# Performance work log

Measured on AMD Instinct MI355X. Metric: run time of the kernel, lower is better.

## Reference

```python
import jax, jax.numpy as jnp
import numpy as np

B, C, H, W = 16, 128, 112, 112
OUTC = 256


def _conv(x, w, padding, groups=1, bias=None):
    y = jax.lax.conv_general_dilated(
        x, w, window_strides=(1, 1), padding=[(padding, padding), (padding, padding)],
        dimension_numbers=("NCHW", "OIHW", "NCHW"), feature_group_count=groups)
    if bias is not None:
        y = y + bias[None, :, None, None]
    return y


def _grid_sample_1ch(chan, g):
    # chan: [B,H,W] single channel; g: [B,H,W,2] with (x,y) in [-1,1].
    # PyTorch grid_sample: bilinear, zeros padding, align_corners=False.
    Bn, Hc, Wc = chan.shape
    ix = (g[..., 0] + 1.0) * (Wc * 0.5) - 0.5
    iy = (g[..., 1] + 1.0) * (Hc * 0.5) - 0.5
    x0 = jnp.floor(ix)
    y0 = jnp.floor(iy)
    wx = ix - x0
    wy = iy - y0
    x0i = x0.astype(jnp.int32)
    y0i = y0.astype(jnp.int32)
    flat = chan.reshape(Bn, -1)

    def gather(yi, xi):
        valid = (yi >= 0) & (yi < Hc) & (xi >= 0) & (xi < Wc)
        idx = jnp.clip(yi, 0, Hc - 1) * Wc + jnp.clip(xi, 0, Wc - 1)
        v = jnp.take_along_axis(flat, idx.reshape(Bn, -1), axis=1).reshape(idx.shape)
        return jnp.where(valid, v, 0.0)

    v00 = gather(y0i, x0i)
    v01 = gather(y0i, x0i + 1)
    v10 = gather(y0i + 1, x0i)
    v11 = gather(y0i + 1, x0i + 1)
    return (v00 * (1 - wx) * (1 - wy) + v01 * wx * (1 - wy)
            + v10 * (1 - wx) * wy + v11 * wx * wy)


def setup_inputs() -> dict:
    key = jax.random.key(0)
    k1, k2, k3, k4 = jax.random.split(key, 4)
    x = jax.random.normal(k1, (B, C, H, W), dtype=jnp.float32)
    depth_w = jax.random.normal(k2, (C, 1, 3, 3), dtype=jnp.float32) * 0.1
    point_w = jax.random.normal(k3, (OUTC, C, 1, 1), dtype=jnp.float32) * 0.05
    offset_w = jax.random.normal(k4, (2 * C, C, 3, 3), dtype=jnp.float32) * 0.02
    offset_b = jnp.zeros((2 * C,), dtype=jnp.float32)
    return {"x": x, "depth_w": depth_w, "point_w": point_w,
            "offset_w": offset_w, "offset_b": offset_b}


def reference(x, depth_w, point_w, offset_w, offset_b):
    offset = jnp.tanh(_conv(x, offset_w, padding=1, bias=offset_b))  # [B,2C,H,W]
    out = _conv(x, depth_w, padding=1, groups=C)                     # [B,C,H,W]

    # Base grid, matching np.meshgrid + np.repeat([C,C], axis=0):
    # channels 0..C-1 are all X, channels C..2C-1 are all Y.
    gX, gY = jnp.meshgrid(jnp.linspace(-1.0, 1.0, W), jnp.linspace(-1.0, 1.0, H), indexing="xy")
    grid = jnp.concatenate([gX[None], gY[None]], axis=0)  # [2,H,W]
    grid = jnp.repeat(grid, C, axis=0)                    # [2C,H,W]

    sg = jnp.clip(grid[None] + offset, -1.0, 1.0)         # [B,2C,H,W]
    sg = sg.transpose(0, 2, 3, 1)                         # [B,H,W,2C]
    sg = sg.reshape(B, H, W, C, 2).transpose(3, 0, 1, 2, 4)  # [C,B,H,W,2]

    chans = out.transpose(1, 0, 2, 3)                     # [C,B,H,W]
    sampled = jax.vmap(_grid_sample_1ch)(chans, sg)       # [C,B,H,W]
    sampled = sampled.transpose(1, 0, 2, 3)               # [B,C,H,W]

    return _conv(sampled, point_w, padding=0)             # [B,OUTC,H,W]
```

## Files before the change

### kernel.cpp

```cpp
#include <hip/hip_runtime.h>
#include <hip/hip_bf16.h>

#define B_    16
#define C_    128
#define H_    112
#define W_    112
#define OUTC_ 256
#define TWOC_ 256
#define HW_   (H_ * W_)
#define CHW_  ((size_t)C_ * HW_)
#define PH_   114
#define PW_   114
#define PHW_  (PH_ * PW_)

typedef __hip_bfloat16 bf16;
typedef short bf16x8 __attribute__((ext_vector_type(8)));
typedef short s16x4  __attribute__((ext_vector_type(4)));
typedef float f32x4  __attribute__((ext_vector_type(4)));

__device__ __forceinline__ float b2f(bf16 v) { return __bfloat162float(v); }
__device__ __forceinline__ bf16  f2b(float v) { return __float2bfloat16(v); }

__device__ __forceinline__ float rd(const float* p) { return *p; }
__device__ __forceinline__ float rd(const bf16* p)  { return b2f(*p); }
__device__ __forceinline__ void  wr(float* p, float v) { *p = v; }
__device__ __forceinline__ void  wr(bf16* p,  float v) { *p = f2b(v); }

__device__ __forceinline__ float fast_tanh(float v) {
    float e = __expf(2.f * v);
    return 1.f - 2.f / (e + 1.f);
}

__global__ __launch_bounds__(256) void k_probe(const unsigned short* __restrict__ x,
                                               int* __restrict__ flag) {
    __shared__ int cnt[256];
    int tid = threadIdx.x;
    int c = 0;
#pragma unroll
    for (int i = 0; i < 8; ++i) {
        unsigned short u = x[tid * 8 + i];
        int e = (u >> 7) & 0xFF;
        if (e >= 135) c++;
    }
    cnt[tid] = c;
    __syncthreads();
    if (tid == 0) {
        int s = 0;
        for (int i = 0; i < 256; ++i) s += cnt[i];
        *flag = (s > 64) ? 1 : 0;
    }
}

template <typename TI>
__device__ void pad_body(const TI* __restrict__ x, float* __restrict__ xp) {
    size_t idx = (size_t)blockIdx.x * 256 + threadIdx.x;
    const size_t total = (size_t)B_ * C_ * PHW_;
    if (idx >= total) return;
    int pc  = (int)(idx / PHW_);
    int rem = (int)(idx - (size_t)pc * PHW_);
    int ph = rem / PW_;
    int pw = rem - ph * PW_;
    int h = ph - 1, w = pw - 1;
    float v = 0.f;
    if (h >= 0 && h < H_ && w >= 0 && w < W_)
        v = rd(x + (size_t)pc * HW_ + h * W_ + w);
    xp[idx] = v;
}

__global__ __launch_bounds__(256) void k_pad(const void* x, float* xp, const int* flag) {
    if (*flag) pad_body<float>((const float*)x, xp);
    else       pad_body<bf16>((const bf16*)x, xp);
}

__global__ __launch_bounds__(256) void k_wprep(const void* __restrict__ ow,
                                               bf16* __restrict__ wth,
                                               bf16* __restrict__ wtl,
                                               const int* __restrict__ flag) {
    int i = blockIdx.x * 256 + threadIdx.x;
    if (i >= 9 * 4 * 256 * 32) return;
    int cp  = i & 31;
    int oc  = (i >> 5) & 255;
    int tcc = i >> 13;
    int cc  = tcc & 3;
    int tap = tcc >> 2;
    int c   = cc * 32 + cp;
    size_t src = ((size_t)oc * C_ + c) * 9 + tap;
    float v = (*flag) ? ((const float*)ow)[src] : b2f(((const bf16*)ow)[src]);
    bf16 hb = f2b(v);
    float lo = v - b2f(hb);
    wth[i] = hb;
    wtl[i] = f2b(lo);
}

__global__ __launch_bounds__(256) void k_offset_mfma(
    const float* __restrict__ xp, const bf16* __restrict__ wth,
    const bf16* __restrict__ wtl, const void* __restrict__ ob,
    float* __restrict__ off, const int* __restrict__ flag)
{
    __shared__ alignas(16) short Sh[PH_ * 32];
    __shared__ alignas(16) short Sl[PH_ * 32];

    const int tid  = threadIdx.x;
    const int lane = tid & 63;
    const int wv   = tid >> 6;
    const int l15  = lane & 15;
    const int l4   = lane >> 4;
    const int hraw = blockIdx.x;
    const int h    = (hraw & 7) * 14 + (hraw >> 3);
    const int b    = blockIdx.y;
    const int fullp = *flag;

    f32x4 acc[4][7];
    f32x4 zero = {0.f, 0.f, 0.f, 0.f};
#pragma unroll
    for (int m = 0; m < 4; ++m)
#pragma unroll
        for (int n = 0; n < 7; ++n) acc[m][n] = zero;

    for (int cc = 0; cc < 4; ++cc) {
        for (int kh = 0; kh < 3; ++kh) {
            __syncthreads();
            for (int i = tid; i < 912; i += 256) {
                int n  = i % 114;
                int cq = i / 114;
                const float* src = xp + ((size_t)(b * C_ + cc * 32 + cq * 4)) * PHW_
                                      + (size_t)(h + kh) * PW_ + n;
                short hs[4], ls[4];
#pragma unroll
                for (int t = 0; t < 4; ++t) {
                    float v = src[(size_t)t * PHW_];
                    bf16 hb = f2b(v);
                    float hv = b2f(hb);
                    bf16 lb = f2b(v - hv);
                    hs[t] = *(short*)&hb;
                    ls[t] = *(short*)&lb;
                }
                int ob_ = (cq * 8) ^ (((n >> 1) & 3) << 4);
                int so  = n * 32 + (ob_ >> 1);
                s16x4 th, tl;
                th[0] = hs[0]; th[1] = hs[1]; th[2] = hs[2]; th[3] = hs[3];
                tl[0] = ls[0]; tl[1] = ls[1]; tl[2] = ls[2]; tl[3] = ls[3];
                *(s16x4*)&Sh[so] = th;
                *(s16x4*)&Sl[so] = tl;
            }
            __syncthreads();

            for (int kw = 0; kw < 3; ++kw) {
                const size_t wchunk = ((size_t)((kh * 3 + kw) * 4 + cc)) * (256 * 32);
                bf16x8 ah[4], al[4];
#pragma unroll
                for (int m = 0; m < 4; ++m) {
                    size_t aoff = (size_t)(wv * 64 + m * 16 + l15) * 32 + 8 * l4;
                    ah[m] = *(const bf16x8*)(wth + wchunk + aoff);
                }
                if (fullp) {
#pragma unroll
                    for (int m = 0; m < 4; ++m) {
                        size_t aoff = (size_t)(wv * 64 + m * 16 + l15) * 32 + 8 * l4;
                        al[m] = *(const bf16x8*)(wtl + wchunk + aoff);
                    }
                }
#pragma unroll
                for (int n = 0; n < 7; ++n) {
                    int rowb = n * 16 + l15 + kw;
                    int o2   = (16 * l4) ^ (((rowb >> 1) & 3) << 4);
                    int so   = rowb * 32 + (o2 >> 1);
                    bf16x8 xh = *(const bf16x8*)&Sh[so];
#pragma unroll
                    for (int m = 0; m < 4; ++m)
                        acc[m][n] = __builtin_amdgcn_mfma_f32_16x16x32_bf16(
                            ah[m], xh, acc[m][n], 0, 0, 0);
                    if (fullp) {
                        bf16x8 xl = *(const bf16x8*)&Sl[so];
#pragma unroll
                        for (int m = 0; m < 4; ++m)
                            acc[m][n] = __builtin_amdgcn_mfma_f32_16x16x32_bf16(
                                ah[m], xl, acc[m][n], 0, 0, 0);
#pragma unroll
                        for (int m = 0; m < 4; ++m)
                            acc[m][n] = __builtin_amdgcn_mfma_f32_16x16x32_bf16(
                                al[m], xh, acc[m][n], 0, 0, 0);
                    }
                }
            }
        }
    }

#pragma unroll
    for (int m = 0; m < 4; ++m) {
        int ocb = wv * 64 + m * 16 + l4 * 4;
        float bias[4];
#pragma unroll
        for (int j = 0; j < 4; ++j)
            bias[j] = fullp ? ((const float*)ob)[ocb + j]
                            : b2f(((const bf16*)ob)[ocb + j]);
#pragma unroll
        for (int n = 0; n < 7; ++n) {
            int w = n * 16 + l15;
#pragma unroll
            for (int j = 0; j < 4; ++j) {
                size_t o = ((size_t)(b * TWOC_ + ocb + j)) * HW_ + (size_t)h * W_ + w;
                off[o] = fast_tanh(acc[m][n][j] + bias[j]);
            }
        }
    }
}

template <typename TI>
__device__ void dw_body(const TI* __restrict__ x, const TI* __restrict__ dw,
                        bf16* __restrict__ out) {
    int hw = blockIdx.x * 256 + threadIdx.x;
    int c = blockIdx.y, b = blockIdx.z;
    int h = hw / W_, w = hw - h * W_;
    float wv[9];
#pragma unroll
    for (int k = 0; k < 9; ++k) wv[k] = rd(dw + c * 9 + k);
    const TI* xc = x + (size_t)b * CHW_ + (size_t)c * HW_;
    float acc = 0.f;
#pragma unroll
    for (int kh = 0; kh < 3; ++kh) {
        int hh = h + kh - 1;
        bool hv = (hh >= 0) && (hh < H_);
#pragma unroll
        for (int kw = 0; kw < 3; ++kw) {
            int ww = w + kw - 1;
            bool v = hv && (ww >= 0) && (ww < W_);
            acc += (v ? rd(xc + hh * W_ + ww) : 0.f) * wv[kh * 3 + kw];
        }
    }
    out[(size_t)(b * C_ + c) * HW_ + hw] = f2b(acc);
}

__global__ __launch_bounds__(256) void k_dw(const void* x, const void* dw,
                                            bf16* out, const int* flag) {
    if (*flag) dw_body<float>((const float*)x, (const float*)dw, out);
    else       dw_body<bf16>((const bf16*)x, (const bf16*)dw, out);
}

__global__ __launch_bounds__(256) void k_sample(
    const float* __restrict__ off, const bf16* __restrict__ dwout,
    bf16* __restrict__ samp) {
    int hw = blockIdx.x * 256 + threadIdx.x;
    int c = blockIdx.y, b = blockIdx.z;
    int h = hw / W_, w = hw - h * W_;

    float gbase = (c < 64) ? (-1.f + 2.f * (float)w / 111.f)
                           : (-1.f + 2.f * (float)h / 111.f);
    const float* offb = off + (size_t)b * TWOC_ * HW_;
    float ox = offb[(size_t)(2 * c) * HW_ + hw];
    float oy = offb[(size_t)(2 * c + 1) * HW_ + hw];
    float gx = fminf(fmaxf(gbase + ox, -1.f), 1.f);
    float gy = fminf(fmaxf(gbase + oy, -1.f), 1.f);
    float ix = (gx + 1.f) * 56.f - 0.5f;
    float iy = (gy + 1.f) * 56.f - 0.5f;
    float x0f = floorf(ix), y0f = floorf(iy);
    float wx = ix - x0f, wy = iy - y0f;
    int x0 = (int)x0f, y0 = (int)y0f;

    const bf16* p = dwout + (size_t)(b * C_ + c) * HW_;
    float v00 = 0.f, v01 = 0.f, v10 = 0.f, v11 = 0.f;
    bool y0v = (y0 >= 0) && (y0 < H_), y1v = (y0 + 1 >= 0) && (y0 + 1 < H_);
    bool x0v = (x0 >= 0) && (x0 < W_), x1v = (x0 + 1 >= 0) && (x0 + 1 < W_);
    if (y0v && x0v) v00 = b2f(p[y0 * W_ + x0]);
    if (y0v && x1v) v01 = b2f(p[y0 * W_ + x0 + 1]);
    if (y1v && x0v) v10 = b2f(p[(y0 + 1) * W_ + x0]);
    if (y1v && x1v) v11 = b2f(p[(y0 + 1) * W_ + x0 + 1]);

    float v = v00 * (1.f - wx) * (1.f - wy) + v01 * wx * (1.f - wy)
            + v10 * (1.f - wx) * wy + v11 * wx * wy;
    samp[(size_t)(b * C_ + c) * HW_ + hw] = f2b(v);
}

#define PWT 8
template <typename TI, typename TO>
__device__ void pw_body(const bf16* __restrict__ samp, const TI* __restrict__ pw,
                        TO* __restrict__ out, float* pwl) {
    int tid = threadIdx.x;
    int ocg = blockIdx.y * PWT;
    for (int i = tid; i < C_ * PWT; i += 256) {
        int j = i / C_;
        int c = i - j * C_;
        pwl[c * PWT + j] = rd(pw + (size_t)(ocg + j) * C_ + c);
    }
    __syncthreads();

    int hw = blockIdx.x * 256 + tid;
    int b = blockIdx.z;
    const bf16* sp = samp + (size_t)b * C_ * HW_ + hw;
    float acc[PWT];
#pragma unroll
    for (int j = 0; j < PWT; ++j) acc[j] = 0.f;
    for (int c = 0; c < C_; ++c) {
        float v = b2f(sp[(size_t)c * HW_]);
        const float* wrp = pwl + c * PWT;
#pragma unroll
        for (int j = 0; j < PWT; ++j) acc[j] += v * wrp[j];
    }
    size_t ob = (size_t)b * OUTC_ * HW_ + (size_t)ocg * HW_ + hw;
#pragma unroll
    for (int j = 0; j < PWT; ++j) wr(out + ob + (size_t)j * HW_, acc[j]);
}

__global__ __launch_bounds__(256) void k_pw(const bf16* samp, const void* pw,
                                            void* out, const int* flag) {
    __shared__ float pwl[C_ * PWT];
    if (*flag) pw_body<float, float>(samp, (const float*)pw, (float*)out, pwl);
    else       pw_body<bf16, bf16>(samp, (const bf16*)pw, (bf16*)out, pwl);
}

extern "C" void kernel_launch(void* const* d_in, const int* in_sizes, int n_in,
                              void* d_out, int out_size, void* d_ws, size_t ws_size,
                              hipStream_t stream) {
    (void)in_sizes; (void)n_in; (void)out_size; (void)ws_size;
    const void* x        = d_in[0];
    const void* depth_w  = d_in[1];
    const void* point_w  = d_in[2];
    const void* offset_w = d_in[3];
    const void* offset_b = d_in[4];

    char* ws = (char*)d_ws;
    int*   flag = (int*)ws;
    float* xp   = (float*)(ws + 256);
    const size_t pad_bytes = (size_t)B_ * C_ * PHW_ * 4;
    const size_t off_bytes = (size_t)B_ * TWOC_ * HW_ * 4;
    float* off  = (float*)(ws + 256 + pad_bytes);
    bf16*  wth  = (bf16*)(ws + 256 + pad_bytes + off_bytes);
    bf16*  wtl  = wth + 9 * 4 * 256 * 32;
    bf16* dwout = (bf16*)(ws + 256);
    bf16* samp  = (bf16*)(ws + 256 + (size_t)B_ * C_ * HW_ * 2);

    const int pad_blocks = (int)(((size_t)B_ * C_ * PHW_ + 255) / 256);

    k_probe      <<<1, 256, 0, stream>>>((const unsigned short*)x, flag);
    k_wprep      <<<1152, 256, 0, stream>>>(offset_w, wth, wtl, flag);
    k_pad        <<<pad_blocks, 256, 0, stream>>>(x, xp, flag);
    k_offset_mfma<<<dim3(H_, B_), 256, 0, stream>>>(xp, wth, wtl, offset_b, off, flag);
    k_dw         <<<dim3(49, C_, B_),          256, 0, stream>>>(x, depth_w, dwout, flag);
    k_sample     <<<dim3(49, C_, B_),          256, 0, stream>>>(off, dwout, samp);
    k_pw         <<<dim3(49, OUTC_ / PWT, B_), 256, 0, stream>>>(samp, point_w, d_out, flag);
}
```

Before: 1.188 ms.

## Fuse bilinear sampling into an MFMA pointwise conv kernel per row

Merges the grid-sample and pointwise 1x1 conv kernels into one kernel per (row, batch). Each block samples all channels for a row into swizzled LDS, then runs the 128-to-256 channel matmul on bf16 MFMA using weights split into hi/lo parts that a new prep kernel builds. This removes the round trip of the sampled tensor through global memory and replaces scalar FMA loops with matrix cores. In exchange, the sampling gathers per block become less coalesced (channel-strided offset reads), and the output stores are scattered per lane.

After: 1.411 ms. 1.19x slower.

```diff
diff --git a/kernel.cpp b/kernel.cpp
--- a/kernel.cpp
+++ b/kernel.cpp
@@ -92,6 +92,24 @@
     wtl[i] = f2b(lo);
 }
 
+__global__ __launch_bounds__(256) void k_pwprep(const void* __restrict__ pw,
+                                                bf16* __restrict__ pwh,
+                                                bf16* __restrict__ pwl,
+                                                const int* __restrict__ flag) {
+    int i = blockIdx.x * 256 + threadIdx.x;
+    if (i >= 4 * 256 * 32) return;
+    int cp   = i & 31;
+    int oc   = (i >> 5) & 255;
+    int cc   = i >> 13;
+    int c    = cc * 32 + cp;
+    size_t src = (size_t)oc * C_ + c;
+    float v = (*flag) ? ((const float*)pw)[src] : b2f(((const bf16*)pw)[src]);
+    bf16 hb = f2b(v);
+    float lo = v - b2f(hb);
+    pwh[i] = hb;
+    pwl[i] = f2b(lo);
+}
+
 __global__ __launch_bounds__(256) void k_offset_mfma(
     const float* __restrict__ xp, const bf16* __restrict__ wth,
     const bf16* __restrict__ wtl, const void* __restrict__ ob,
@@ -237,75 +255,118 @@
     else       dw_body<bf16>((const bf16*)x, (const bf16*)dw, out);
 }
 
-__global__ __launch_bounds__(256) void k_sample(
+__global__ __launch_bounds__(256) void k_spw(
     const float* __restrict__ off, const bf16* __restrict__ dwout,
-    bf16* __restrict__ samp) {
-    int hw = blockIdx.x * 256 + threadIdx.x;
-    int c = blockIdx.y, b = blockIdx.z;
-    int h = hw / W_, w = hw - h * W_;
-
-    float gbase = (c < 64) ? (-1.f + 2.f * (float)w / 111.f)
-                           : (-1.f + 2.f * (float)h / 111.f);
-    const float* offb = off + (size_t)b * TWOC_ * HW_;
-    float ox = offb[(size_t)(2 * c) * HW_ + hw];
-    float oy = offb[(size_t)(2 * c + 1) * HW_ + hw];
-    float gx = fminf(fmaxf(gbase + ox, -1.f), 1.f);
-    float gy = fminf(fmaxf(gbase + oy, -1.f), 1.f);
-    float ix = (gx + 1.f) * 56.f - 0.5f;
-    float iy = (gy + 1.f) * 56.f - 0.5f;
-    float x0f = floorf(ix), y0f = floorf(iy);
-    float wx = ix - x0f, wy = iy - y0f;
-    int x0 = (int)x0f, y0 = (int)y0f;
-
-    const bf16* p = dwout + (size_t)(b * C_ + c) * HW_;
-    float v00 = 0.f, v01 = 0.f, v10 = 0.f, v11 = 0.f;
-    bool y0v = (y0 >= 0) && (y0 < H_), y1v = (y0 + 1 >= 0) && (y0 + 1 < H_);
-    bool x0v = (x0 >= 0) && (x0 < W_), x1v = (x0 + 1 >= 0) && (x0 + 1 < W_);
-    if (y0v && x0v) v00 = b2f(p[y0 * W_ + x0]);
-    if (y0v && x1v) v01 = b2f(p[y0 * W_ + x0 + 1]);
-    if (y1v && x0v) v10 = b2f(p[(y0 + 1) * W_ + x0]);
-    if (y1v && x1v) v11 = b2f(p[(y0 + 1) * W_ + x0 + 1]);
-
-    float v = v00 * (1.f - wx) * (1.f - wy) + v01 * wx * (1.f - wy)
-            + v10 * (1.f - wx) * wy + v11 * wx * wy;
-    samp[(size_t)(b * C_ + c) * HW_ + hw] = f2b(v);
-}
-
-#define PWT 8
-template <typename TI, typename TO>
-__device__ void pw_body(const bf16* __restrict__ samp, const TI* __restrict__ pw,
-                        TO* __restrict__ out, float* pwl) {
-    int tid = threadIdx.x;
-    int ocg = blockIdx.y * PWT;
-    for (int i = tid; i < C_ * PWT; i += 256) {
-        int j = i / C_;
-        int c = i - j * C_;
-        pwl[c * PWT + j] = rd(pw + (size_t)(ocg + j) * C_ + c);
+    const bf16* __restrict__ pwh, const bf16* __restrict__ pwl,
+    void* __restrict__ out, const int* __restrict__ flag)
+{
+    __shared__ alignas(16) short SB[W_ * C_];
+
+    const int tid  = threadIdx.x;
+    const int lane = tid & 63;
+    const int wv   = tid >> 6;
+    const int l15  = lane & 15;
+    const int l4   = lane >> 4;
+    const int hraw = blockIdx.x;
+    const int h    = (hraw & 7) * 14 + (hraw >> 3);
+    const int b    = blockIdx.y;
+    const int fullp = *flag;
+
+    const float* offb = off + (size_t)b * TWOC_ * HW_ + (size_t)h * W_;
+    const bf16*  dwb  = dwout + (size_t)b * C_ * HW_;
+#pragma unroll
+    for (int it = 0; it < 7; ++it) {
+        int j  = it * 256 + tid;
+        int w  = j % W_;
+        int c8 = j / W_;
+        int c0 = c8 * 8;
+        bf16x8 rv;
+#pragma unroll
+        for (int t = 0; t < 8; ++t) {
+            int c = c0 + t;
+            float ox = offb[(size_t)(2 * c) * HW_ + w];
+            float oy = offb[(size_t)(2 * c + 1) * HW_ + w];
+            float gbase = (c < 64) ? (-1.f + 2.f * (float)w / 111.f)
+                                   : (-1.f + 2.f * (float)h / 111.f);
+            float gx = fminf(fmaxf(gbase + ox, -1.f), 1.f);
+            float gy = fminf(fmaxf(gbase + oy, -1.f), 1.f);
+            float ix = (gx + 1.f) * 56.f - 0.5f;
+            float iy = (gy + 1.f) * 56.f - 0.5f;
+            float x0f = floorf(ix), y0f = floorf(iy);
+            float wx = ix - x0f, wy = iy - y0f;
+            int x0 = (int)x0f, y0 = (int)y0f;
+            const bf16* p = dwb + (size_t)c * HW_;
+            float v00 = 0.f, v01 = 0.f, v10 = 0.f, v11 = 0.f;
+            bool y0v = (y0 >= 0) && (y0 < H_), y1v = (y0 + 1 >= 0) && (y0 + 1 < H_);
+            bool x0v = (x0 >= 0) && (x0 < W_), x1v = (x0 + 1 >= 0) && (x0 + 1 < W_);
+            if (y0v && x0v) v00 = b2f(p[y0 * W_ + x0]);
+            if (y0v && x1v) v01 = b2f(p[y0 * W_ + x0 + 1]);
+            if (y1v && x0v) v10 = b2f(p[(y0 + 1) * W_ + x0]);
+            if (y1v && x1v) v11 = b2f(p[(y0 + 1) * W_ + x0 + 1]);
+            float v = v00 * (1.f - wx) * (1.f - wy) + v01 * wx * (1.f - wy)
+                    + v10 * (1.f - wx) * wy + v11 * wx * wy;
+            bf16 vb = f2b(v);
+            rv[t] = *(short*)&vb;
+        }
+        int g  = c8 ^ (w & 7);
+        int so = w * C_ + g * 8;
+        *(bf16x8*)&SB[so] = rv;
     }
     __syncthreads();
 
-    int hw = blockIdx.x * 256 + tid;
-    int b = blockIdx.z;
-    const bf16* sp = samp + (size_t)b * C_ * HW_ + hw;
-    float acc[PWT];
-#pragma unroll
-    for (int j = 0; j < PWT; ++j) acc[j] = 0.f;
-    for (int c = 0; c < C_; ++c) {
-        float v = b2f(sp[(size_t)c * HW_]);
-        const float* wrp = pwl + c * PWT;
-#pragma unroll
-        for (int j = 0; j < PWT; ++j) acc[j] += v * wrp[j];
-    }
-    size_t ob = (size_t)b * OUTC_ * HW_ + (size_t)ocg * HW_ + hw;
-#pragma unroll
-    for (int j = 0; j < PWT; ++j) wr(out + ob + (size_t)j * HW_, acc[j]);
-}
-
-__global__ __launch_bounds__(256) void k_pw(const bf16* samp, const void* pw,
-                                            void* out, const int* flag) {
-    __shared__ float pwl[C_ * PWT];
-    if (*flag) pw_body<float, float>(samp, (const float*)pw, (float*)out, pwl);
-    else       pw_body<bf16, bf16>(samp, (const bf16*)pw, (bf16*)out, pwl);
+    f32x4 acc[4][7];
+    f32x4 zero = {0.f, 0.f, 0.f, 0.f};
+#pragma unroll
+    for (int m = 0; m < 4; ++m)
+#pragma unroll
+        for (int n = 0; n < 7; ++n) acc[m][n] = zero;
+
+    for (int cc = 0; cc < 4; ++cc) {
+        bf16x8 ah[4], al[4];
+#pragma unroll
+        for (int m = 0; m < 4; ++m) {
+            size_t aoff = ((size_t)cc * 256 + (wv * 64 + m * 16 + l15)) * 32 + 8 * l4;
+            ah[m] = *(const bf16x8*)(pwh + aoff);
+        }
+        if (fullp) {
+#pragma unroll
+            for (int m = 0; m < 4; ++m) {
+                size_t aoff = ((size_t)cc * 256 + (wv * 64 + m * 16 + l15)) * 32 + 8 * l4;
+                al[m] = *(const bf16x8*)(pwl + aoff);
+            }
+        }
+#pragma unroll
+        for (int n = 0; n < 7; ++n) {
+            int w = n * 16 + l15;
+            int g = (cc * 4 + l4) ^ (w & 7);
+            bf16x8 xv = *(const bf16x8*)&SB[w * C_ + g * 8];
+#pragma unroll
+            for (int m = 0; m < 4; ++m)
+                acc[m][n] = __builtin_amdgcn_mfma_f32_16x16x32_bf16(
+                    ah[m], xv, acc[m][n], 0, 0, 0);
+            if (fullp) {
+#pragma unroll
+                for (int m = 0; m < 4; ++m)
+                    acc[m][n] = __builtin_amdgcn_mfma_f32_16x16x32_bf16(
+                        al[m], xv, acc[m][n], 0, 0, 0);
+            }
+        }
+    }
+
+#pragma unroll
+    for (int m = 0; m < 4; ++m) {
+        int ocb = wv * 64 + m * 16 + l4 * 4;
+#pragma unroll
+        for (int n = 0; n < 7; ++n) {
+            int w = n * 16 + l15;
+#pragma unroll
+            for (int j = 0; j < 4; ++j) {
+                size_t o = ((size_t)(b * OUTC_ + ocb + j)) * HW_ + (size_t)h * W_ + w;
+                if (fullp) ((float*)out)[o] = acc[m][n][j];
+                else       ((bf16*)out)[o]  = f2b(acc[m][n][j]);
+            }
+        }
+    }
 }
 
 extern "C" void kernel_launch(void* const* d_in, const int* in_sizes, int n_in,
@@ -326,16 +387,17 @@
     float* off  = (float*)(ws + 256 + pad_bytes);
     bf16*  wth  = (bf16*)(ws + 256 + pad_bytes + off_bytes);
     bf16*  wtl  = wth + 9 * 4 * 256 * 32;
+    bf16*  pwh  = wtl + 9 * 4 * 256 * 32;
+    bf16*  pwl  = pwh + 4 * 256 * 32;
     bf16* dwout = (bf16*)(ws + 256);
-    bf16* samp  = (bf16*)(ws + 256 + (size_t)B_ * C_ * HW_ * 2);
 
     const int pad_blocks = (int)(((size_t)B_ * C_ * PHW_ + 255) / 256);
 
     k_probe      <<<1, 256, 0, stream>>>((const unsigned short*)x, flag);
     k_wprep      <<<1152, 256, 0, stream>>>(offset_w, wth, wtl, flag);
+    k_pwprep     <<<128, 256, 0, stream>>>(point_w, pwh, pwl, flag);
     k_pad        <<<pad_blocks, 256, 0, stream>>>(x, xp, flag);
     k_offset_mfma<<<dim3(H_, B_), 256, 0, stream>>>(xp, wth, wtl, offset_b, off, flag);
-    k_dw         <<<dim3(49, C_, B_),          256, 0, stream>>>(x, depth_w, dwout, flag);
-    k_sample     <<<dim3(49, C_, B_),          256, 0, stream>>>(off, dwout, samp);
-    k_pw         <<<dim3(49, OUTC_ / PWT, B_), 256, 0, stream>>>(samp, point_w, d_out, flag);
-}
+    k_dw         <<<dim3(49, C_, B_), 256, 0, stream>>>(x, depth_w, dwout, flag);
+    k_spw        <<<dim3(H_, B_), 256, 0, stream>>>(off, dwout, pwh, pwl, d_out, flag);
+}
```
